# Kernel optimization log

Measured on AMD Instinct MI355X. Metric: run time of the kernel, lower is better.

Reference implementation:

```python
import jax, jax.numpy as jnp
import numpy as np

D = 2048        # input_size / model dim
H = 2816        # hidden_size per expert (GLU -> w1 has 2*H rows)
E = 8           # num_experts
M = 4096        # tokens (batch*seq)


def setup_inputs() -> dict:
    key = jax.random.key(0)
    k1, k2, k3, k4, k5 = jax.random.split(key, 5)
    x = jax.random.normal(k1, (M, D), dtype=jnp.float32)
    # ParallelExperts init: uniform(-1/fan_in_dim, 1/fan_in_dim); scale kept simple here
    w1 = jax.random.uniform(k2, (E, 2 * H, D), dtype=jnp.float32, minval=-1.0, maxval=1.0) / (2 * H)
    w2 = jax.random.uniform(k3, (E, D, H), dtype=jnp.float32, minval=-1.0, maxval=1.0) / D
    router_w = jax.random.normal(k4, (E, D), dtype=jnp.float32) * (1.0 / np.sqrt(D))
    bias = jnp.zeros((D,), dtype=jnp.float32)
    return {"x": x, "w1": w1, "w2": w2, "router_w": router_w, "bias": bias, "top_k": 2}


def _moe_forward(x, w1, w2, router_w, bias, top_k):
    # Router: logits -> softmax (fp32) -> top-k -> renormalize (fused_moe semantics)
    logits = x @ router_w.T                                # [M, E]
    probs = jax.nn.softmax(logits.astype(jnp.float32), axis=-1)
    topk_w, topk_ids = jax.lax.top_k(probs, top_k)         # [M, k]
    topk_w = topk_w / jnp.sum(topk_w, axis=-1, keepdims=True)
    # Dense combine weights [M, E]: gate weight if expert selected, else 0
    m = x.shape[0]
    combine = jnp.zeros((m, w1.shape[0]), dtype=x.dtype)
    combine = combine.at[jnp.arange(m)[:, None], topk_ids].add(topk_w.astype(x.dtype))
    # Grouped expert GEMMs, expressed as a loop over the small fixed expert set.
    # Contribution of expert e is masked by combine[:, e] (zero for unrouted tokens).
    y = jnp.zeros_like(x)
    hdim = w2.shape[2]
    for e in range(w1.shape[0]):
        g = x @ w1[e].T                                    # [M, 2H]
        h = jax.nn.silu(g[:, :hdim]) * g[:, hdim:]          # silu_and_mul (GLU)
        y = y + combine[:, e:e + 1] * (h @ w2[e].T)         # [M, D]
    return y + bias


def reference(x, w1, w2, router_w, bias, top_k):
    return _moe_forward(x, w1, w2, router_w, bias, top_k)
```

## Files before the change

kernel.cpp:

```cpp
#include <hip/hip_runtime.h>
#include <hip/hip_bf16.h>
#include <stdint.h>

#define M_TOK 4096
#define DDIM  2048
#define HDIM  2816
#define NEXP  8
#define PMAX  10240
#define MAXTILES 40
#define NB1   22
#define NB2   8
#define NKT1  32
#define NKT2  44

typedef __attribute__((ext_vector_type(8))) short short8;
typedef __attribute__((ext_vector_type(4))) float f32x4;

#define GLD16(g, l) __builtin_amdgcn_global_load_lds(                              \
    (const __attribute__((address_space(1))) unsigned int*)(g),                    \
    (__attribute__((address_space(3))) unsigned int*)(l), 16, 0, 0)

#define VMCNT(n) asm volatile("s_waitcnt vmcnt(" #n ")" ::: "memory")

__device__ __forceinline__ unsigned short f2bf(float f) {
  unsigned int u = __float_as_uint(f);
  u += 0x7fffu + ((u >> 16) & 1u);
  return (unsigned short)(u >> 16);
}
__device__ __forceinline__ float bf2f(unsigned short u) {
  return __uint_as_float(((unsigned)u) << 16);
}


#define STGA(TT, PP, S)                                                            \
  { size_t kb_ = (size_t)(TT) * 128 + (S) * 64;                                    \
    char* d_ = ldsp + (PP) * 32768 + (S) * 16384;                                  \
    GLD16(aS0 + kb_, d_ + tid * 16); GLD16(aS1 + kb_, d_ + 8192 + tid * 16); }

#define STGB(TT, PP, S)                                                            \
  { size_t kb_ = (size_t)(TT) * 128 + (S) * 64;                                    \
    char* d_ = ldsp + 65536 + (PP) * 32768 + (S) * 16384;                          \
    GLD16(bS0 + kb_, d_ + tid * 16); GLD16(bS1 + kb_, d_ + 8192 + tid * 16); }

#define DSRA(PP, S, M)                                                             \
  { const char* ab_ = ldsp + (PP) * 32768 + (S) * 16384;                           \
    _Pragma("unroll") for (int j_ = 0; j_ < 4; ++j_)                               \
      av[j_] = *(const short8*)(ab_ + aoff[(M) * 4 + j_]); }

#define DSRB(PP, S)                                                                \
  { const char* bb_ = ldsp + 65536 + (PP) * 32768 + (S) * 16384;                   \
    _Pragma("unroll") for (int j_ = 0; j_ < 4; ++j_)                               \
      bv[j_] = *(const short8*)(bb_ + boff[j_]); }

#define MMA16(M)                                                                   \
  { __builtin_amdgcn_s_setprio(1);                                                 \
    _Pragma("unroll") for (int j_ = 0; j_ < 4; ++j_)                               \
      _Pragma("unroll") for (int n_ = 0; n_ < 4; ++n_)                             \
        acc[(M) * 4 + j_][n_] =                                                    \
          __builtin_amdgcn_mfma_f32_16x16x32_bf16(av[j_], bv[n_], acc[(M)*4+j_][n_], 0, 0, 0); \
    __builtin_amdgcn_s_setprio(0); }

#define KTILE(T, P, S0, S1, S2, S3, VM)                                            \
  {                       \
    DSRA(P, 0, 0); DSRB(P, 0);                                                     \
    if (S0) STGA((T) + 1, (P) ^ 1, 1);                                             \
    __builtin_amdgcn_s_barrier(); MMA16(0); __builtin_amdgcn_s_barrier();          \
                          \
    DSRA(P, 0, 1);                                                                 \
    if (S1) STGB((T) + 2, P, 0);                                                   \
    __builtin_amdgcn_s_barrier(); MMA16(1); __builtin_amdgcn_s_barrier();          \
                          \
    DSRA(P, 1, 0); DSRB(P, 1);                                                     \
    if (S2) STGA((T) + 2, P, 0);                                                   \
    __builtin_amdgcn_s_barrier(); MMA16(0); __builtin_amdgcn_s_barrier();          \
        \
    DSRA(P, 1, 1);                                                                 \
    if (S3) STGB((T) + 2, P, 1);                                                   \
    __builtin_amdgcn_s_barrier(); MMA16(1);                                        \
    VMCNT(VM);                                                                     \
    __builtin_amdgcn_s_barrier(); }

__global__ void cvt_bf16_k(const float4* __restrict__ in, ushort4* __restrict__ out, int n4) {
  int stride = gridDim.x * blockDim.x;
  for (int i = blockIdx.x * blockDim.x + threadIdx.x; i < n4; i += stride) {
    float4 v = in[i];
    ushort4 o;
    o.x = f2bf(v.x); o.y = f2bf(v.y); o.z = f2bf(v.z); o.w = f2bf(v.w);
    out[i] = o;
  }
}

__global__ void init_k(int* __restrict__ tok, int* __restrict__ counts, int* __restrict__ cursors) {
  int i = blockIdx.x * blockDim.x + threadIdx.x;
  if (i < PMAX) tok[i] = -1;
  if (i < NEXP) { counts[i] = 0; cursors[i] = 0; }
}

__global__ __launch_bounds__(256) void router_k(const float4* __restrict__ x4,
                                                const float4* __restrict__ rw4,
                                                ushort4* __restrict__ xb4,
                                                float* __restrict__ wgt,
                                                int* __restrict__ eid,
                                                int* __restrict__ counts) {
  int lane = threadIdx.x & 63;
  int wv = threadIdx.x >> 6;
  int t = blockIdx.x * 4 + wv;
  int base = t * (DDIM / 4);
  float acc[NEXP];
#pragma unroll
  for (int e = 0; e < NEXP; ++e) acc[e] = 0.f;
#pragma unroll
  for (int j = 0; j < DDIM / 4 / 64; ++j) {
    float4 v = x4[base + j * 64 + lane];
    ushort4 o;
    o.x = f2bf(v.x); o.y = f2bf(v.y); o.z = f2bf(v.z); o.w = f2bf(v.w);
    xb4[base + j * 64 + lane] = o;
#pragma unroll
    for (int e = 0; e < NEXP; ++e) {
      float4 w = rw4[e * (DDIM / 4) + j * 64 + lane];
      acc[e] += v.x * w.x + v.y * w.y + v.z * w.z + v.w * w.w;
    }
  }
#pragma unroll
  for (int e = 0; e < NEXP; ++e) {
#pragma unroll
    for (int s = 32; s > 0; s >>= 1) acc[e] += __shfl_xor(acc[e], s, 64);
  }
  if (lane == 0) {
    float mx = acc[0];
#pragma unroll
    for (int e = 1; e < NEXP; ++e) mx = fmaxf(mx, acc[e]);
    float p[NEXP];
#pragma unroll
    for (int e = 0; e < NEXP; ++e) p[e] = expf(acc[e] - mx);
    int e0 = 0; float p0 = p[0];
#pragma unroll
    for (int e = 1; e < NEXP; ++e) if (p[e] > p0) { p0 = p[e]; e0 = e; }
    int e1 = -1; float p1 = -1.f;
#pragma unroll
    for (int e = 0; e < NEXP; ++e) if (e != e0 && p[e] > p1) { p1 = p[e]; e1 = e; }
    float s = p0 + p1;
    wgt[2 * t] = p0 / s; wgt[2 * t + 1] = p1 / s;
    eid[2 * t] = e0;     eid[2 * t + 1] = e1;
    atomicAdd(&counts[e0], 1);
    atomicAdd(&counts[e1], 1);
  }
}

__global__ void offsets_k(const int* __restrict__ counts, int* __restrict__ offs,
                          int* __restrict__ tile2exp, int* __restrict__ tilerow,
                          int* __restrict__ ntiles) {
  if (threadIdx.x == 0 && blockIdx.x == 0) {
    int o = 0, nt = 0;
    for (int e = 0; e < NEXP; ++e) {
      offs[e] = o;
      int c = counts[e];
      int pt = (c + 255) >> 8;
      for (int i = 0; i < pt; ++i) { tile2exp[nt] = e; tilerow[nt] = o + i * 256; ++nt; }
      o += pt << 8;
    }
    offs[NEXP] = o;
    ntiles[0] = nt;
  }
}

__global__ void scatter_k(const int* __restrict__ eid, const int* __restrict__ offs,
                          int* __restrict__ cursors, int* __restrict__ tok,
                          int* __restrict__ slot) {
  int t = blockIdx.x * blockDim.x + threadIdx.x;
  if (t >= M_TOK) return;
#pragma unroll
  for (int k = 0; k < 2; ++k) {
    int e = eid[2 * t + k];
    int p = offs[e] + atomicAdd(&cursors[e], 1);
    tok[p] = t;
    slot[2 * t + k] = p;
  }
}

__global__ __launch_bounds__(512, 1) void gemm1_k(const unsigned short* __restrict__ xb,
                                                  const unsigned short* __restrict__ w1b,
                                                  const int* __restrict__ tok,
                                                  const int* __restrict__ tile2exp,
                                                  const int* __restrict__ tilerow,
                                                  const int* __restrict__ ntiles,
                                                  unsigned short* __restrict__ h) {
  __shared__ char ldsp[131072];
  int mt = blockIdx.x;
  if (mt >= ntiles[0]) return;
  int e = tile2exp[mt], r0 = tilerow[mt];
  int n0 = blockIdx.y * 128;
  int tid = threadIdx.x, lane = tid & 63;
  int wv = tid >> 6, wm = wv >> 2, wn = wv & 3;
  int l15 = lane & 15, g = lane >> 4;

  int row0 = tid >> 2, g0 = (tid & 3) ^ ((row0 >> 1) & 3);
  int row1 = row0 + 128;
  int t0 = tok[r0 + row0]; if (t0 < 0) t0 = 0;
  int t1 = tok[r0 + row1]; if (t1 < 0) t1 = 0;
  const char* aS0 = (const char*)xb + (size_t)t0 * (DDIM * 2) + g0 * 16;
  const char* aS1 = (const char*)xb + (size_t)t1 * (DDIM * 2) + g0 * 16;
  size_t w1r0 = (size_t)e * (2 * HDIM) + (size_t)(n0 + row0);
  size_t w1r1 = (size_t)e * (2 * HDIM) + (size_t)(HDIM + n0 + row0);
  const char* bS0 = (const char*)w1b + w1r0 * (DDIM * 2) + g0 * 16;
  const char* bS1 = (const char*)w1b + w1r1 * (DDIM * 2) + g0 * 16;

  int aoff[8], boff[4];
#pragma unroll
  for (int mi = 0; mi < 8; ++mi) {
    int r = wm * 128 + mi * 16 + l15;
    aoff[mi] = r * 64 + ((g ^ ((r >> 1) & 3)) << 4);
  }
#pragma unroll
  for (int ni = 0; ni < 4; ++ni) {
    int r = wn * 64 + ni * 16 + l15;
    boff[ni] = r * 64 + ((g ^ ((r >> 1) & 3)) << 4);
  }

  f32x4 acc[8][4];
#pragma unroll
  for (int mi = 0; mi < 8; ++mi)
#pragma unroll
    for (int ni = 0; ni < 4; ++ni) acc[mi][ni] = (f32x4)(0.f);

  short8 av[4], bv[4];

  STGA(0, 0, 0); STGB(0, 0, 0); STGA(0, 0, 1); STGB(0, 0, 1);
  STGB(1, 1, 0); STGA(1, 1, 0); STGB(1, 1, 1);
  VMCNT(6);
  __builtin_amdgcn_s_barrier();

#pragma unroll 1
  for (int t = 0; t < NKT1 - 2; t += 2) {
    KTILE(t, 0, 1, 1, 1, 1, 6);
    KTILE(t + 1, 1, 1, 1, 1, 1, 6);
  }
  KTILE(NKT1 - 2, 0, 1, 0, 0, 0, 0);
  KTILE(NKT1 - 1, 1, 0, 0, 0, 0, 0);

  __syncthreads();
  float* xch = (float*)ldsp;
  int rbase = (lane >> 4) * 4;
  if (wn >= 2) {
    int uc0 = (wn - 2) * 64;
#pragma unroll
    for (int mi = 0; mi < 8; ++mi)
#pragma unroll
      for (int ni = 0; ni < 4; ++ni)
#pragma unroll
        for (int j = 0; j < 4; ++j) {
          int r = wm * 128 + mi * 16 + rbase + j;
          int c = uc0 + ni * 16 + l15;
          int cs = c ^ ((r & 3) << 2) ^ ((r & 1) << 4);
          xch[r * 128 + cs] = acc[mi][ni][j];
        }
  }
  __syncthreads();
  if (wn < 2) {
#pragma unroll
    for (int mi = 0; mi < 8; ++mi)
#pragma unroll
      for (int ni = 0; ni < 4; ++ni)
#pragma unroll
        for (int j = 0; j < 4; ++j) {
          int r = wm * 128 + mi * 16 + rbase + j;
          int c = wn * 64 + ni * 16 + l15;
          int cs = c ^ ((r & 3) << 2) ^ ((r & 1) << 4);
          float gg = acc[mi][ni][j];
          float u = xch[r * 128 + cs];
          float sv = gg / (1.f + expf(-gg));
          h[(size_t)(r0 + r) * HDIM + n0 + c] = f2bf(sv * u);
        }
  }
}

__global__ __launch_bounds__(512, 1) void gemm2_k(const unsigned short* __restrict__ h,
                                                  const unsigned short* __restrict__ w2b,
                                                  const int* __restrict__ tile2exp,
                                                  const int* __restrict__ tilerow,
                                                  const int* __restrict__ ntiles,
                                                  unsigned short* __restrict__ yp) {
  __shared__ char ldsp[131072];
  int mt = blockIdx.x;
  if (mt >= ntiles[0]) return;
  int e = tile2exp[mt], r0 = tilerow[mt];
  int n0 = blockIdx.y * 256;
  int tid = threadIdx.x, lane = tid & 63;
  int wv = tid >> 6, wm = wv >> 2, wn = wv & 3;
  int l15 = lane & 15, g = lane >> 4;

  int row0 = tid >> 2, g0 = (tid & 3) ^ ((row0 >> 1) & 3);
  int row1 = row0 + 128;
  const char* aS0 = (const char*)h + (size_t)(r0 + row0) * (HDIM * 2) + g0 * 16;
  const char* aS1 = (const char*)h + (size_t)(r0 + row1) * (HDIM * 2) + g0 * 16;
  const char* bS0 = (const char*)w2b + ((size_t)e * DDIM + n0 + row0) * (HDIM * 2) + g0 * 16;
  const char* bS1 = (const char*)w2b + ((size_t)e * DDIM + n0 + row1) * (HDIM * 2) + g0 * 16;

  int aoff[8], boff[4];
#pragma unroll
  for (int mi = 0; mi < 8; ++mi) {
    int r = wm * 128 + mi * 16 + l15;
    aoff[mi] = r * 64 + ((g ^ ((r >> 1) & 3)) << 4);
  }
#pragma unroll
  for (int ni = 0; ni < 4; ++ni) {
    int r = wn * 64 + ni * 16 + l15;
    boff[ni] = r * 64 + ((g ^ ((r >> 1) & 3)) << 4);
  }

  f32x4 acc[8][4];
#pragma unroll
  for (int mi = 0; mi < 8; ++mi)
#pragma unroll
    for (int ni = 0; ni < 4; ++ni) acc[mi][ni] = (f32x4)(0.f);

  short8 av[4], bv[4];

  STGA(0, 0, 0); STGB(0, 0, 0); STGA(0, 0, 1); STGB(0, 0, 1);
  STGB(1, 1, 0); STGA(1, 1, 0); STGB(1, 1, 1);
  VMCNT(6);
  __builtin_amdgcn_s_barrier();

#pragma unroll 1
  for (int t = 0; t < NKT2 - 2; t += 2) {
    KTILE(t, 0, 1, 1, 1, 1, 6);
    KTILE(t + 1, 1, 1, 1, 1, 1, 6);
  }
  KTILE(NKT2 - 2, 0, 1, 0, 0, 0, 0);
  KTILE(NKT2 - 1, 1, 0, 0, 0, 0, 0);

  int rbase = (lane >> 4) * 4;
#pragma unroll
  for (int mi = 0; mi < 8; ++mi)
#pragma unroll
    for (int ni = 0; ni < 4; ++ni)
#pragma unroll
      for (int j = 0; j < 4; ++j) {
        int r = r0 + wm * 128 + mi * 16 + rbase + j;
        int c = n0 + wn * 64 + ni * 16 + l15;
        yp[(size_t)r * DDIM + c] = f2bf(acc[mi][ni][j]);
      }
}

__global__ void combine_k(const unsigned short* __restrict__ yp, const float* __restrict__ wgt,
                          const int* __restrict__ slot, const float* __restrict__ bias,
                          float* __restrict__ out) {
  int idx = blockIdx.x * blockDim.x + threadIdx.x;
  int t = idx >> 8, q = (idx & 255) * 8;
  float w0 = wgt[2 * t], w1 = wgt[2 * t + 1];
  int s0 = slot[2 * t], s1 = slot[2 * t + 1];
  short8 a8 = *(const short8*)(yp + (size_t)s0 * DDIM + q);
  short8 b8 = *(const short8*)(yp + (size_t)s1 * DDIM + q);
  float* op = out + (size_t)t * DDIM + q;
#pragma unroll
  for (int k = 0; k < 8; ++k) {
    float av = bf2f((unsigned short)a8[k]);
    float bv = bf2f((unsigned short)b8[k]);
    op[k] = w0 * av + w1 * bv + bias[q + k];
  }
}

extern "C" void kernel_launch(void* const* d_in, const int* in_sizes, int n_in,
                              void* d_out, int out_size, void* d_ws, size_t ws_size,
                              hipStream_t stream) {
  const float* x    = (const float*)d_in[0];
  const float* w1   = (const float*)d_in[1];
  const float* w2   = (const float*)d_in[2];
  const float* rw   = (const float*)d_in[3];
  const float* bias = (const float*)d_in[4];
  float* out = (float*)d_out;

  char* ws = (char*)d_ws;
  size_t off = 0;
  auto alloc = [&](size_t bytes) -> void* {
    void* p = ws + off;
    off = (off + bytes + 255) & ~(size_t)255;
    return p;
  };
  unsigned short* w1b = (unsigned short*)alloc((size_t)NEXP * 2 * HDIM * DDIM * 2);
  unsigned short* w2b = (unsigned short*)alloc((size_t)NEXP * DDIM * HDIM * 2);
  unsigned short* xb  = (unsigned short*)alloc((size_t)M_TOK * DDIM * 2);
  unsigned short* h   = (unsigned short*)alloc((size_t)PMAX * HDIM * 2);
  unsigned short* yp  = (unsigned short*)alloc((size_t)PMAX * DDIM * 2);
  float* wgt          = (float*)alloc((size_t)M_TOK * 2 * 4);
  int* eid            = (int*)alloc((size_t)M_TOK * 2 * 4);
  int* slot           = (int*)alloc((size_t)M_TOK * 2 * 4);
  int* tok            = (int*)alloc((size_t)PMAX * 4);
  int* counts         = (int*)alloc(64 * 4);
  int* cursors        = (int*)alloc(64 * 4);
  int* offs           = (int*)alloc(64 * 4);
  int* ntiles         = (int*)alloc(64 * 4);
  int* tile2exp       = (int*)alloc(128 * 4);
  int* tilerow        = (int*)alloc(128 * 4);

  hipLaunchKernelGGL(init_k, dim3((PMAX + 255) / 256), dim3(256), 0, stream, tok, counts, cursors);
  hipLaunchKernelGGL(cvt_bf16_k, dim3(2048), dim3(256), 0, stream,
                     (const float4*)w1, (ushort4*)w1b, (int)((size_t)NEXP * 2 * HDIM * DDIM / 4));
  hipLaunchKernelGGL(cvt_bf16_k, dim3(2048), dim3(256), 0, stream,
                     (const float4*)w2, (ushort4*)w2b, (int)((size_t)NEXP * DDIM * HDIM / 4));
  hipLaunchKernelGGL(router_k, dim3(M_TOK / 4), dim3(256), 0, stream,
                     (const float4*)x, (const float4*)rw, (ushort4*)xb, wgt, eid, counts);
  hipLaunchKernelGGL(offsets_k, dim3(1), dim3(64), 0, stream, counts, offs,
                     tile2exp, tilerow, ntiles);
  hipLaunchKernelGGL(scatter_k, dim3((M_TOK + 255) / 256), dim3(256), 0, stream, eid, offs, cursors, tok, slot);
  hipLaunchKernelGGL(gemm1_k, dim3(MAXTILES, NB1), dim3(512), 0, stream,
                     xb, w1b, tok, tile2exp, tilerow, ntiles, h);
  hipLaunchKernelGGL(gemm2_k, dim3(MAXTILES, NB2), dim3(512), 0, stream,
                     h, w2b, tile2exp, tilerow, ntiles, yp);
  hipLaunchKernelGGL(combine_k, dim3(M_TOK * (DDIM / 8) / 256), dim3(256), 0, stream, yp, wgt, slot, bias, out);
}
```

Baseline: 750.6 us.

## Halve gemm2 M-tile to 128 rows with a 4-stage pipeline, merge weight conversions

The second grouped GEMM now uses 128x256 output tiles instead of 256x256, with a separate tile list so twice as many blocks are launched. It switches to a 4-deep LDS ring with K-step 32 and double-buffered register fragments, so LDS reads for the next step overlap the MFMAs of the current one. The goal is better CU occupancy for the small total tile count and less exposed latency. The cost is less reuse of w2 per block, which means more weight traffic. The two fp32-to-bf16 weight conversion launches are also merged into one kernel to save a launch.

```diff
diff --git a/kernel.cpp b/kernel.cpp
--- a/kernel.cpp
+++ b/kernel.cpp
@@ -9,9 +9,10 @@
 #define PMAX  10240
 #define MAXTILES 40
 #define NB1   22
+#define MAXT2 80
 #define NB2   8
 #define NKT1  32
-#define NKT2  44
+#define NT2   88
 
 typedef __attribute__((ext_vector_type(8))) short short8;
 typedef __attribute__((ext_vector_type(4))) float f32x4;
@@ -30,7 +31,6 @@
 __device__ __forceinline__ float bf2f(unsigned short u) {
   return __uint_as_float(((unsigned)u) << 16);
 }
-
 
 #define STGA(TT, PP, S)                                                            \
   { size_t kb_ = (size_t)(TT) * 128 + (S) * 64;                                    \
@@ -61,32 +61,31 @@
     __builtin_amdgcn_s_setprio(0); }
 
 #define KTILE(T, P, S0, S1, S2, S3, VM)                                            \
-  {                       \
-    DSRA(P, 0, 0); DSRB(P, 0);                                                     \
+  { DSRA(P, 0, 0); DSRB(P, 0);                                                     \
     if (S0) STGA((T) + 1, (P) ^ 1, 1);                                             \
     __builtin_amdgcn_s_barrier(); MMA16(0); __builtin_amdgcn_s_barrier();          \
-                          \
     DSRA(P, 0, 1);                                                                 \
     if (S1) STGB((T) + 2, P, 0);                                                   \
     __builtin_amdgcn_s_barrier(); MMA16(1); __builtin_amdgcn_s_barrier();          \
-                          \
     DSRA(P, 1, 0); DSRB(P, 1);                                                     \
     if (S2) STGA((T) + 2, P, 0);                                                   \
     __builtin_amdgcn_s_barrier(); MMA16(0); __builtin_amdgcn_s_barrier();          \
-        \
     DSRA(P, 1, 1);                                                                 \
     if (S3) STGB((T) + 2, P, 1);                                                   \
     __builtin_amdgcn_s_barrier(); MMA16(1);                                        \
     VMCNT(VM);                                                                     \
     __builtin_amdgcn_s_barrier(); }
 
-__global__ void cvt_bf16_k(const float4* __restrict__ in, ushort4* __restrict__ out, int n4) {
+__global__ void cvt2_bf16_k(const float4* __restrict__ in1, ushort4* __restrict__ out1, int n1,
+                            const float4* __restrict__ in2, ushort4* __restrict__ out2, int n2) {
   int stride = gridDim.x * blockDim.x;
-  for (int i = blockIdx.x * blockDim.x + threadIdx.x; i < n4; i += stride) {
-    float4 v = in[i];
+  for (int i = blockIdx.x * blockDim.x + threadIdx.x; i < n1 + n2; i += stride) {
+    const float4* ip; ushort4* op; int j;
+    if (i < n1) { ip = in1; op = out1; j = i; } else { ip = in2; op = out2; j = i - n1; }
+    float4 v = ip[j];
     ushort4 o;
     o.x = f2bf(v.x); o.y = f2bf(v.y); o.z = f2bf(v.z); o.w = f2bf(v.w);
-    out[i] = o;
+    op[j] = o;
   }
 }
 
@@ -149,18 +148,25 @@
 
 __global__ void offsets_k(const int* __restrict__ counts, int* __restrict__ offs,
                           int* __restrict__ tile2exp, int* __restrict__ tilerow,
-                          int* __restrict__ ntiles) {
+                          int* __restrict__ ntiles,
+                          int* __restrict__ tile2exp2, int* __restrict__ tilerow2,
+                          int* __restrict__ ntiles2) {
   if (threadIdx.x == 0 && blockIdx.x == 0) {
-    int o = 0, nt = 0;
+    int o = 0, nt = 0, nt2 = 0;
     for (int e = 0; e < NEXP; ++e) {
       offs[e] = o;
       int c = counts[e];
       int pt = (c + 255) >> 8;
-      for (int i = 0; i < pt; ++i) { tile2exp[nt] = e; tilerow[nt] = o + i * 256; ++nt; }
+      for (int i = 0; i < pt; ++i) {
+        tile2exp[nt] = e; tilerow[nt] = o + i * 256; ++nt;
+        tile2exp2[nt2] = e; tilerow2[nt2] = o + i * 256; ++nt2;
+        tile2exp2[nt2] = e; tilerow2[nt2] = o + i * 256 + 128; ++nt2;
+      }
       o += pt << 8;
     }
     offs[NEXP] = o;
     ntiles[0] = nt;
+    ntiles2[0] = nt2;
   }
 }
 
@@ -274,69 +280,105 @@
   }
 }
 
+#define STAGE2(TT)                                                               \
+  { size_t kb_ = (size_t)(TT) * 64;                                              \
+    GLD16(aS0 + kb_, ldsp + ((TT) & 3) * 8192 + aD0);                            \
+    GLD16(bS0 + kb_, ldsp + 32768 + ((TT) & 3) * 16384 + bD0);                   \
+    GLD16(bS1 + kb_, ldsp + 32768 + ((TT) & 3) * 16384 + bD1); }
+
+#define DSRD2(TT, AV, BV)                                                        \
+  { const char* ab_ = ldsp + ((TT) & 3) * 8192;                                  \
+    const char* bb_ = ldsp + 32768 + ((TT) & 3) * 16384;                         \
+    _Pragma("unroll") for (int mi = 0; mi < 4; ++mi)                             \
+      AV[mi] = *(const short8*)(ab_ + aoff[mi]);                                 \
+    _Pragma("unroll") for (int ni = 0; ni < 4; ++ni)                             \
+      BV[ni] = *(const short8*)(bb_ + boff[ni]); }
+
+#define MMA2(AV, BV)                                                             \
+  { __builtin_amdgcn_s_setprio(1);                                               \
+    _Pragma("unroll") for (int mi = 0; mi < 4; ++mi)                             \
+      _Pragma("unroll") for (int ni = 0; ni < 4; ++ni)                           \
+        acc[mi][ni] = __builtin_amdgcn_mfma_f32_16x16x32_bf16(AV[mi], BV[ni], acc[mi][ni], 0, 0, 0); \
+    __builtin_amdgcn_s_setprio(0); }
+
+#define BODY2(TT, VMN, STG, AVC, BVC, AVN, BVN, RD)                              \
+  { VMCNT(VMN);                                                                  \
+    __builtin_amdgcn_s_barrier();                                                \
+    asm volatile("" ::: "memory");                                               \
+    if (STG) STAGE2((TT) + 3);                                                   \
+    if (RD) DSRD2((TT) + 1, AVN, BVN);                                           \
+    __builtin_amdgcn_sched_barrier(0);                                           \
+    MMA2(AVC, BVC); }
+
 __global__ __launch_bounds__(512, 1) void gemm2_k(const unsigned short* __restrict__ h,
                                                   const unsigned short* __restrict__ w2b,
-                                                  const int* __restrict__ tile2exp,
-                                                  const int* __restrict__ tilerow,
-                                                  const int* __restrict__ ntiles,
+                                                  const int* __restrict__ tile2exp2,
+                                                  const int* __restrict__ tilerow2,
+                                                  const int* __restrict__ ntiles2,
                                                   unsigned short* __restrict__ yp) {
-  __shared__ char ldsp[131072];
+  __shared__ char ldsp[98304];
   int mt = blockIdx.x;
-  if (mt >= ntiles[0]) return;
-  int e = tile2exp[mt], r0 = tilerow[mt];
+  if (mt >= ntiles2[0]) return;
+  int e = tile2exp2[mt], r0 = tilerow2[mt];
   int n0 = blockIdx.y * 256;
   int tid = threadIdx.x, lane = tid & 63;
   int wv = tid >> 6, wm = wv >> 2, wn = wv & 3;
   int l15 = lane & 15, g = lane >> 4;
 
-  int row0 = tid >> 2, g0 = (tid & 3) ^ ((row0 >> 1) & 3);
-  int row1 = row0 + 128;
-  const char* aS0 = (const char*)h + (size_t)(r0 + row0) * (HDIM * 2) + g0 * 16;
-  const char* aS1 = (const char*)h + (size_t)(r0 + row1) * (HDIM * 2) + g0 * 16;
-  const char* bS0 = (const char*)w2b + ((size_t)e * DDIM + n0 + row0) * (HDIM * 2) + g0 * 16;
-  const char* bS1 = (const char*)w2b + ((size_t)e * DDIM + n0 + row1) * (HDIM * 2) + g0 * 16;
-
-  int aoff[8], boff[4];
-#pragma unroll
-  for (int mi = 0; mi < 8; ++mi) {
-    int r = wm * 128 + mi * 16 + l15;
-    aoff[mi] = r * 64 + ((g ^ ((r >> 1) & 3)) << 4);
+  int rowa = tid >> 2, ga = (tid & 3) ^ ((rowa >> 1) & 3);
+  int rb0 = tid >> 2, gb0 = (tid & 3) ^ ((rb0 >> 1) & 3);
+  int s1i = 512 + tid;
+  int rb1 = s1i >> 2, gb1 = (s1i & 3) ^ ((rb1 >> 1) & 3);
+  const char* aS0 = (const char*)h + (size_t)(r0 + rowa) * (HDIM * 2) + ga * 16;
+  const char* bS0 = (const char*)w2b + ((size_t)e * DDIM + n0 + rb0) * (HDIM * 2) + gb0 * 16;
+  const char* bS1 = (const char*)w2b + ((size_t)e * DDIM + n0 + rb1) * (HDIM * 2) + gb1 * 16;
+  int aD0 = tid * 16, bD0 = tid * 16, bD1 = 8192 + tid * 16;
+
+  int aoff[4], boff[4];
+#pragma unroll
+  for (int mi = 0; mi < 4; ++mi) {
+    int r = wm * 64 + mi * 16 + l15;
+    aoff[mi] = r * 64 + ((g ^ ((r >> 1) & 3)) * 16);
   }
 #pragma unroll
   for (int ni = 0; ni < 4; ++ni) {
     int r = wn * 64 + ni * 16 + l15;
-    boff[ni] = r * 64 + ((g ^ ((r >> 1) & 3)) << 4);
-  }
-
-  f32x4 acc[8][4];
-#pragma unroll
-  for (int mi = 0; mi < 8; ++mi)
+    boff[ni] = r * 64 + ((g ^ ((r >> 1) & 3)) * 16);
+  }
+
+  f32x4 acc[4][4];
+#pragma unroll
+  for (int mi = 0; mi < 4; ++mi)
 #pragma unroll
     for (int ni = 0; ni < 4; ++ni) acc[mi][ni] = (f32x4)(0.f);
 
-  short8 av[4], bv[4];
-
-  STGA(0, 0, 0); STGB(0, 0, 0); STGA(0, 0, 1); STGB(0, 0, 1);
-  STGB(1, 1, 0); STGA(1, 1, 0); STGB(1, 1, 1);
+  short8 avA[4], bvA[4], avB[4], bvB[4];
+
+  STAGE2(0); STAGE2(1); STAGE2(2);
   VMCNT(6);
   __builtin_amdgcn_s_barrier();
-
-#pragma unroll 1
-  for (int t = 0; t < NKT2 - 2; t += 2) {
-    KTILE(t, 0, 1, 1, 1, 1, 6);
-    KTILE(t + 1, 1, 1, 1, 1, 1, 6);
-  }
-  KTILE(NKT2 - 2, 0, 1, 0, 0, 0, 0);
-  KTILE(NKT2 - 1, 1, 0, 0, 0, 0, 0);
+  asm volatile("" ::: "memory");
+  DSRD2(0, avA, bvA);
+
+  for (int T = 0; T < NT2 - 4; T += 4) {
+    BODY2(T + 0, 3, 1, avA, bvA, avB, bvB, 1);
+    BODY2(T + 1, 3, 1, avB, bvB, avA, bvA, 1);
+    BODY2(T + 2, 3, 1, avA, bvA, avB, bvB, 1);
+    BODY2(T + 3, 3, 1, avB, bvB, avA, bvA, 1);
+  }
+  BODY2(NT2 - 4, 3, 1, avA, bvA, avB, bvB, 1);
+  BODY2(NT2 - 3, 3, 0, avB, bvB, avA, bvA, 1);
+  BODY2(NT2 - 2, 0, 0, avA, bvA, avB, bvB, 1);
+  BODY2(NT2 - 1, 0, 0, avB, bvB, avA, bvA, 0);
 
   int rbase = (lane >> 4) * 4;
 #pragma unroll
-  for (int mi = 0; mi < 8; ++mi)
+  for (int mi = 0; mi < 4; ++mi)
 #pragma unroll
     for (int ni = 0; ni < 4; ++ni)
 #pragma unroll
       for (int j = 0; j < 4; ++j) {
-        int r = r0 + wm * 128 + mi * 16 + rbase + j;
+        int r = r0 + wm * 64 + mi * 16 + rbase + j;
         int c = n0 + wn * 64 + ni * 16 + l15;
         yp[(size_t)r * DDIM + c] = f2bf(acc[mi][ni][j]);
       }
@@ -390,22 +432,24 @@
   int* cursors        = (int*)alloc(64 * 4);
   int* offs           = (int*)alloc(64 * 4);
   int* ntiles         = (int*)alloc(64 * 4);
+  int* ntiles2        = (int*)alloc(64 * 4);
   int* tile2exp       = (int*)alloc(128 * 4);
   int* tilerow        = (int*)alloc(128 * 4);
+  int* tile2exp2      = (int*)alloc(128 * 4);
+  int* tilerow2       = (int*)alloc(128 * 4);
 
   hipLaunchKernelGGL(init_k, dim3((PMAX + 255) / 256), dim3(256), 0, stream, tok, counts, cursors);
-  hipLaunchKernelGGL(cvt_bf16_k, dim3(2048), dim3(256), 0, stream,
-                     (const float4*)w1, (ushort4*)w1b, (int)((size_t)NEXP * 2 * HDIM * DDIM / 4));
-  hipLaunchKernelGGL(cvt_bf16_k, dim3(2048), dim3(256), 0, stream,
+  hipLaunchKernelGGL(cvt2_bf16_k, dim3(2048), dim3(256), 0, stream,
+                     (const float4*)w1, (ushort4*)w1b, (int)((size_t)NEXP * 2 * HDIM * DDIM / 4),
                      (const float4*)w2, (ushort4*)w2b, (int)((size_t)NEXP * DDIM * HDIM / 4));
   hipLaunchKernelGGL(router_k, dim3(M_TOK / 4), dim3(256), 0, stream,
                      (const float4*)x, (const float4*)rw, (ushort4*)xb, wgt, eid, counts);
   hipLaunchKernelGGL(offsets_k, dim3(1), dim3(64), 0, stream, counts, offs,
-                     tile2exp, tilerow, ntiles);
+                     tile2exp, tilerow, ntiles, tile2exp2, tilerow2, ntiles2);
   hipLaunchKernelGGL(scatter_k, dim3((M_TOK + 255) / 256), dim3(256), 0, stream, eid, offs, cursors, tok, slot);
   hipLaunchKernelGGL(gemm1_k, dim3(MAXTILES, NB1), dim3(512), 0, stream,
                      xb, w1b, tok, tile2exp, tilerow, ntiles, h);
-  hipLaunchKernelGGL(gemm2_k, dim3(MAXTILES, NB2), dim3(512), 0, stream,
-                     h, w2b, tile2exp, tilerow, ntiles, yp);
+  hipLaunchKernelGGL(gemm2_k, dim3(MAXT2, NB2), dim3(512), 0, stream,
+                     h, w2b, tile2exp2, tilerow2, ntiles2, yp);
   hipLaunchKernelGGL(combine_k, dim3(M_TOK * (DDIM / 8) / 256), dim3(256), 0, stream, yp, wgt, slot, bias, out);
 }
```

New measurement: 754.4 us. No clear change (+0.5%).

## Simplify GEMM pipeline to full-K-tile double buffering and fuse conversion kernels

Applied to the files above, without the earlier changes.

Replaces the interleaved half-tile staging schedule in both expert GEMMs with a simple double-buffered loop that loads a full 128-byte K slice per stage and uses an 8-way XOR swizzle with 128-byte LDS rows. Each stage now issues all eight async loads, waits, then runs all 32 MFMAs per half-slice from one set of LDS reads, with fewer barriers. The two weight conversion kernels and the init kernel are merged into one launch that also unrolls its grid-stride loop by two. The aim is lower barrier and launch overhead, at the risk of weaker load/compute overlap than the finer-grained previous schedule.

```diff
diff --git a/kernel.cpp b/kernel.cpp
--- a/kernel.cpp
+++ b/kernel.cpp
@@ -31,69 +31,32 @@
   return __uint_as_float(((unsigned)u) << 16);
 }
 
-
-#define STGA(TT, PP, S)                                                            \
-  { size_t kb_ = (size_t)(TT) * 128 + (S) * 64;                                    \
-    char* d_ = ldsp + (PP) * 32768 + (S) * 16384;                                  \
-    GLD16(aS0 + kb_, d_ + tid * 16); GLD16(aS1 + kb_, d_ + 8192 + tid * 16); }
-
-#define STGB(TT, PP, S)                                                            \
-  { size_t kb_ = (size_t)(TT) * 128 + (S) * 64;                                    \
-    char* d_ = ldsp + 65536 + (PP) * 32768 + (S) * 16384;                          \
-    GLD16(bS0 + kb_, d_ + tid * 16); GLD16(bS1 + kb_, d_ + 8192 + tid * 16); }
-
-#define DSRA(PP, S, M)                                                             \
-  { const char* ab_ = ldsp + (PP) * 32768 + (S) * 16384;                           \
-    _Pragma("unroll") for (int j_ = 0; j_ < 4; ++j_)                               \
-      av[j_] = *(const short8*)(ab_ + aoff[(M) * 4 + j_]); }
-
-#define DSRB(PP, S)                                                                \
-  { const char* bb_ = ldsp + 65536 + (PP) * 32768 + (S) * 16384;                   \
-    _Pragma("unroll") for (int j_ = 0; j_ < 4; ++j_)                               \
-      bv[j_] = *(const short8*)(bb_ + boff[j_]); }
-
-#define MMA16(M)                                                                   \
-  { __builtin_amdgcn_s_setprio(1);                                                 \
-    _Pragma("unroll") for (int j_ = 0; j_ < 4; ++j_)                               \
-      _Pragma("unroll") for (int n_ = 0; n_ < 4; ++n_)                             \
-        acc[(M) * 4 + j_][n_] =                                                    \
-          __builtin_amdgcn_mfma_f32_16x16x32_bf16(av[j_], bv[n_], acc[(M)*4+j_][n_], 0, 0, 0); \
-    __builtin_amdgcn_s_setprio(0); }
-
-#define KTILE(T, P, S0, S1, S2, S3, VM)                                            \
-  {                       \
-    DSRA(P, 0, 0); DSRB(P, 0);                                                     \
-    if (S0) STGA((T) + 1, (P) ^ 1, 1);                                             \
-    __builtin_amdgcn_s_barrier(); MMA16(0); __builtin_amdgcn_s_barrier();          \
-                          \
-    DSRA(P, 0, 1);                                                                 \
-    if (S1) STGB((T) + 2, P, 0);                                                   \
-    __builtin_amdgcn_s_barrier(); MMA16(1); __builtin_amdgcn_s_barrier();          \
-                          \
-    DSRA(P, 1, 0); DSRB(P, 1);                                                     \
-    if (S2) STGA((T) + 2, P, 0);                                                   \
-    __builtin_amdgcn_s_barrier(); MMA16(0); __builtin_amdgcn_s_barrier();          \
-        \
-    DSRA(P, 1, 1);                                                                 \
-    if (S3) STGB((T) + 2, P, 1);                                                   \
-    __builtin_amdgcn_s_barrier(); MMA16(1);                                        \
-    VMCNT(VM);                                                                     \
-    __builtin_amdgcn_s_barrier(); }
-
-__global__ void cvt_bf16_k(const float4* __restrict__ in, ushort4* __restrict__ out, int n4) {
-  int stride = gridDim.x * blockDim.x;
-  for (int i = blockIdx.x * blockDim.x + threadIdx.x; i < n4; i += stride) {
-    float4 v = in[i];
+__global__ void cvt2_bf16_k(const float4* __restrict__ in1, ushort4* __restrict__ out1, int n1,
+                            const float4* __restrict__ in2, ushort4* __restrict__ out2, int n2,
+                            int* __restrict__ tok, int* __restrict__ counts,
+                            int* __restrict__ cursors) {
+  int gid = blockIdx.x * blockDim.x + threadIdx.x;
+  if (gid < PMAX) tok[gid] = -1;
+  if (gid < NEXP) { counts[gid] = 0; cursors[gid] = 0; }
+  const int stride = gridDim.x * blockDim.x;
+  const int total = n1 + n2;
+  int i = gid;
+  for (; i + stride < total; i += 2 * stride) {
+    int ia = i, ib = i + stride;
+    float4 va = (ia < n1) ? in1[ia] : in2[ia - n1];
+    float4 vb = (ib < n1) ? in1[ib] : in2[ib - n1];
+    ushort4 oa, ob;
+    oa.x = f2bf(va.x); oa.y = f2bf(va.y); oa.z = f2bf(va.z); oa.w = f2bf(va.w);
+    ob.x = f2bf(vb.x); ob.y = f2bf(vb.y); ob.z = f2bf(vb.z); ob.w = f2bf(vb.w);
+    if (ia < n1) out1[ia] = oa; else out2[ia - n1] = oa;
+    if (ib < n1) out1[ib] = ob; else out2[ib - n1] = ob;
+  }
+  if (i < total) {
+    float4 v = (i < n1) ? in1[i] : in2[i - n1];
     ushort4 o;
     o.x = f2bf(v.x); o.y = f2bf(v.y); o.z = f2bf(v.z); o.w = f2bf(v.w);
-    out[i] = o;
-  }
-}
-
-__global__ void init_k(int* __restrict__ tok, int* __restrict__ counts, int* __restrict__ cursors) {
-  int i = blockIdx.x * blockDim.x + threadIdx.x;
-  if (i < PMAX) tok[i] = -1;
-  if (i < NEXP) { counts[i] = 0; cursors[i] = 0; }
+    if (i < n1) out1[i] = o; else out2[i - n1] = o;
+  }
 }
 
 __global__ __launch_bounds__(256) void router_k(const float4* __restrict__ x4,
@@ -178,6 +141,31 @@
   }
 }
 
+
+#define STG8(KT, D)                                                                \
+  { size_t kb_ = (size_t)(KT) * 128;                                               \
+    char* Ad_ = ldsp + (D) * 32768 + tid * 16;                                     \
+    char* Bd_ = ldsp + 65536 + (D) * 32768 + tid * 16;                             \
+    _Pragma("unroll") for (int u_ = 0; u_ < 4; ++u_) {                             \
+      GLD16(aSrc[u_] + kb_, Ad_ + u_ * 8192);                                      \
+      GLD16(bSrc[u_] + kb_, Bd_ + u_ * 8192);                                      \
+    } }
+
+#define KBODY(AB, BB)                                                              \
+  _Pragma("unroll") for (int s_ = 0; s_ < 2; ++s_) {                               \
+    short8 a_[8], b_[4];                                                           \
+    int sx_ = s_ << 6;                                                             \
+    _Pragma("unroll") for (int i_ = 0; i_ < 8; ++i_)                               \
+      a_[i_] = *(const short8*)((AB) + (aoff[i_] ^ sx_));                          \
+    _Pragma("unroll") for (int i_ = 0; i_ < 4; ++i_)                               \
+      b_[i_] = *(const short8*)((BB) + (boff[i_] ^ sx_));                          \
+    __builtin_amdgcn_s_setprio(1);                                                 \
+    _Pragma("unroll") for (int mi_ = 0; mi_ < 8; ++mi_)                            \
+      _Pragma("unroll") for (int ni_ = 0; ni_ < 4; ++ni_)                          \
+        acc[mi_][ni_] = __builtin_amdgcn_mfma_f32_16x16x32_bf16(a_[mi_], b_[ni_], acc[mi_][ni_], 0, 0, 0); \
+    __builtin_amdgcn_s_setprio(0);                                                 \
+  }
+
 __global__ __launch_bounds__(512, 1) void gemm1_k(const unsigned short* __restrict__ xb,
                                                   const unsigned short* __restrict__ w1b,
                                                   const int* __restrict__ tok,
@@ -192,29 +180,29 @@
   int n0 = blockIdx.y * 128;
   int tid = threadIdx.x, lane = tid & 63;
   int wv = tid >> 6, wm = wv >> 2, wn = wv & 3;
-  int l15 = lane & 15, g = lane >> 4;
-
-  int row0 = tid >> 2, g0 = (tid & 3) ^ ((row0 >> 1) & 3);
-  int row1 = row0 + 128;
-  int t0 = tok[r0 + row0]; if (t0 < 0) t0 = 0;
-  int t1 = tok[r0 + row1]; if (t1 < 0) t1 = 0;
-  const char* aS0 = (const char*)xb + (size_t)t0 * (DDIM * 2) + g0 * 16;
-  const char* aS1 = (const char*)xb + (size_t)t1 * (DDIM * 2) + g0 * 16;
-  size_t w1r0 = (size_t)e * (2 * HDIM) + (size_t)(n0 + row0);
-  size_t w1r1 = (size_t)e * (2 * HDIM) + (size_t)(HDIM + n0 + row0);
-  const char* bS0 = (const char*)w1b + w1r0 * (DDIM * 2) + g0 * 16;
-  const char* bS1 = (const char*)w1b + w1r1 * (DDIM * 2) + g0 * 16;
+  int l15 = lane & 15, lq = lane >> 4;
+
+  int srow = tid >> 3, sq = tid & 7;
+  const char* aSrc[4]; const char* bSrc[4];
+#pragma unroll
+  for (int u = 0; u < 4; ++u) {
+    int r = srow + u * 64;
+    int t = tok[r0 + r]; if (t < 0) t = 0;
+    aSrc[u] = (const char*)xb + (size_t)t * (DDIM * 2) + ((sq ^ (r & 7)) << 4);
+    int w1row = e * (2 * HDIM) + (r < 128 ? n0 + r : HDIM + n0 + (r - 128));
+    bSrc[u] = (const char*)w1b + (size_t)w1row * (DDIM * 2) + ((sq ^ (r & 7)) << 4);
+  }
 
   int aoff[8], boff[4];
 #pragma unroll
   for (int mi = 0; mi < 8; ++mi) {
     int r = wm * 128 + mi * 16 + l15;
-    aoff[mi] = r * 64 + ((g ^ ((r >> 1) & 3)) << 4);
+    aoff[mi] = r * 128 + ((lq ^ (r & 7)) << 4);
   }
 #pragma unroll
   for (int ni = 0; ni < 4; ++ni) {
     int r = wn * 64 + ni * 16 + l15;
-    boff[ni] = r * 64 + ((g ^ ((r >> 1) & 3)) << 4);
+    boff[ni] = r * 128 + ((lq ^ (r & 7)) << 4);
   }
 
   f32x4 acc[8][4];
@@ -223,24 +211,22 @@
 #pragma unroll
     for (int ni = 0; ni < 4; ++ni) acc[mi][ni] = (f32x4)(0.f);
 
-  short8 av[4], bv[4];
-
-  STGA(0, 0, 0); STGB(0, 0, 0); STGA(0, 0, 1); STGB(0, 0, 1);
-  STGB(1, 1, 0); STGA(1, 1, 0); STGB(1, 1, 1);
-  VMCNT(6);
-  __builtin_amdgcn_s_barrier();
-
+  STG8(0, 0);
 #pragma unroll 1
-  for (int t = 0; t < NKT1 - 2; t += 2) {
-    KTILE(t, 0, 1, 1, 1, 1, 6);
-    KTILE(t + 1, 1, 1, 1, 1, 1, 6);
-  }
-  KTILE(NKT1 - 2, 0, 1, 0, 0, 0, 0);
-  KTILE(NKT1 - 1, 1, 0, 0, 0, 0, 0);
+  for (int kt = 0; kt < NKT1; ++kt) {
+    int d = kt & 1;
+    if (kt + 1 < NKT1) { STG8(kt + 1, d ^ 1); VMCNT(8); }
+    else { VMCNT(0); }
+    __builtin_amdgcn_s_barrier();
+    const char* Ab = ldsp + d * 32768;
+    const char* Bb = ldsp + 65536 + d * 32768;
+    KBODY(Ab, Bb);
+    __builtin_amdgcn_s_barrier();
+  }
 
   __syncthreads();
   float* xch = (float*)ldsp;
-  int rbase = (lane >> 4) * 4;
+  int rbase = lq * 4;
   if (wn >= 2) {
     int uc0 = (wn - 2) * 64;
 #pragma unroll
@@ -287,25 +273,27 @@
   int n0 = blockIdx.y * 256;
   int tid = threadIdx.x, lane = tid & 63;
   int wv = tid >> 6, wm = wv >> 2, wn = wv & 3;
-  int l15 = lane & 15, g = lane >> 4;
-
-  int row0 = tid >> 2, g0 = (tid & 3) ^ ((row0 >> 1) & 3);
-  int row1 = row0 + 128;
-  const char* aS0 = (const char*)h + (size_t)(r0 + row0) * (HDIM * 2) + g0 * 16;
-  const char* aS1 = (const char*)h + (size_t)(r0 + row1) * (HDIM * 2) + g0 * 16;
-  const char* bS0 = (const char*)w2b + ((size_t)e * DDIM + n0 + row0) * (HDIM * 2) + g0 * 16;
-  const char* bS1 = (const char*)w2b + ((size_t)e * DDIM + n0 + row1) * (HDIM * 2) + g0 * 16;
+  int l15 = lane & 15, lq = lane >> 4;
+
+  int srow = tid >> 3, sq = tid & 7;
+  const char* aSrc[4]; const char* bSrc[4];
+#pragma unroll
+  for (int u = 0; u < 4; ++u) {
+    int r = srow + u * 64;
+    aSrc[u] = (const char*)h + (size_t)(r0 + r) * (HDIM * 2) + ((sq ^ (r & 7)) << 4);
+    bSrc[u] = (const char*)w2b + ((size_t)e * DDIM + n0 + r) * (HDIM * 2) + ((sq ^ (r & 7)) << 4);
+  }
 
   int aoff[8], boff[4];
 #pragma unroll
   for (int mi = 0; mi < 8; ++mi) {
     int r = wm * 128 + mi * 16 + l15;
-    aoff[mi] = r * 64 + ((g ^ ((r >> 1) & 3)) << 4);
+    aoff[mi] = r * 128 + ((lq ^ (r & 7)) << 4);
   }
 #pragma unroll
   for (int ni = 0; ni < 4; ++ni) {
     int r = wn * 64 + ni * 16 + l15;
-    boff[ni] = r * 64 + ((g ^ ((r >> 1) & 3)) << 4);
+    boff[ni] = r * 128 + ((lq ^ (r & 7)) << 4);
   }
 
   f32x4 acc[8][4];
@@ -314,22 +302,20 @@
 #pragma unroll
     for (int ni = 0; ni < 4; ++ni) acc[mi][ni] = (f32x4)(0.f);
 
-  short8 av[4], bv[4];
-
-  STGA(0, 0, 0); STGB(0, 0, 0); STGA(0, 0, 1); STGB(0, 0, 1);
-  STGB(1, 1, 0); STGA(1, 1, 0); STGB(1, 1, 1);
-  VMCNT(6);
-  __builtin_amdgcn_s_barrier();
-
+  STG8(0, 0);
 #pragma unroll 1
-  for (int t = 0; t < NKT2 - 2; t += 2) {
-    KTILE(t, 0, 1, 1, 1, 1, 6);
-    KTILE(t + 1, 1, 1, 1, 1, 1, 6);
-  }
-  KTILE(NKT2 - 2, 0, 1, 0, 0, 0, 0);
-  KTILE(NKT2 - 1, 1, 0, 0, 0, 0, 0);
-
-  int rbase = (lane >> 4) * 4;
+  for (int kt = 0; kt < NKT2; ++kt) {
+    int d = kt & 1;
+    if (kt + 1 < NKT2) { STG8(kt + 1, d ^ 1); VMCNT(8); }
+    else { VMCNT(0); }
+    __builtin_amdgcn_s_barrier();
+    const char* Ab = ldsp + d * 32768;
+    const char* Bb = ldsp + 65536 + d * 32768;
+    KBODY(Ab, Bb);
+    __builtin_amdgcn_s_barrier();
+  }
+
+  int rbase = lq * 4;
 #pragma unroll
   for (int mi = 0; mi < 8; ++mi)
 #pragma unroll
@@ -393,11 +379,10 @@
   int* tile2exp       = (int*)alloc(128 * 4);
   int* tilerow        = (int*)alloc(128 * 4);
 
-  hipLaunchKernelGGL(init_k, dim3((PMAX + 255) / 256), dim3(256), 0, stream, tok, counts, cursors);
-  hipLaunchKernelGGL(cvt_bf16_k, dim3(2048), dim3(256), 0, stream,
-                     (const float4*)w1, (ushort4*)w1b, (int)((size_t)NEXP * 2 * HDIM * DDIM / 4));
-  hipLaunchKernelGGL(cvt_bf16_k, dim3(2048), dim3(256), 0, stream,
-                     (const float4*)w2, (ushort4*)w2b, (int)((size_t)NEXP * DDIM * HDIM / 4));
+  hipLaunchKernelGGL(cvt2_bf16_k, dim3(4096), dim3(256), 0, stream,
+                     (const float4*)w1, (ushort4*)w1b, (int)((size_t)NEXP * 2 * HDIM * DDIM / 4),
+                     (const float4*)w2, (ushort4*)w2b, (int)((size_t)NEXP * DDIM * HDIM / 4),
+                     tok, counts, cursors);
   hipLaunchKernelGGL(router_k, dim3(M_TOK / 4), dim3(256), 0, stream,
                      (const float4*)x, (const float4*)rw, (ushort4*)xb, wgt, eid, counts);
   hipLaunchKernelGGL(offsets_k, dim3(1), dim3(64), 0, stream, counts, offs,
```

Result: slower. 793.2 us (+5.7%).
